# Kernel tuning notes

Measured on AMD Instinct MI355X. Metric: run time of the kernel, lower is better.

Reference implementation:

```python
import math
import jax, jax.numpy as jnp
import numpy as np

NEG = -1e10


def _rope_cos_sin(T, head_dim, dtype):
    # theta_i = 10000^(-2*(i-1)/dim), i=1..dim/2  ->  j=0..dim/2-1: 10000^(-2j/dim)
    j = jnp.arange(head_dim // 2, dtype=jnp.float32)
    inv_freq = 1.0 / (10000.0 ** (2.0 * j / head_dim))
    t = jnp.arange(T, dtype=jnp.float32)
    ang = t[:, None] * inv_freq[None, :]          # [T, hd/2]
    return jnp.cos(ang).astype(dtype), jnp.sin(ang).astype(dtype)


def _apply_rope(x, cos, sin):
    # x: [B, H, T, hd]; complex multiply (cos + i sin) * (x0 + i x1)
    B, H, T, hd = x.shape
    xr = x.reshape(B, H, T, hd // 2, 2)
    x0, x1 = xr[..., 0], xr[..., 1]
    c = cos[None, None]  # [1,1,T,hd/2]
    s = sin[None, None]
    o0 = c * x0 - s * x1
    o1 = s * x0 + c * x1
    return jnp.stack([o0, o1], axis=-1).reshape(B, H, T, hd)


def setup_inputs() -> dict:
    key = jax.random.key(0)
    ks = jax.random.split(key, 9)
    B, T, C = 2, 2048, 1024
    std = 0.02
    return {
        "x": jax.random.normal(ks[0], (B, T, C), jnp.float32),
        "Wq": jax.random.normal(ks[1], (C, C), jnp.float32) * std,
        "bq": jnp.zeros((C,), jnp.float32),
        "Wk": jax.random.normal(ks[2], (C, C), jnp.float32) * std,
        "bk": jnp.zeros((C,), jnp.float32),
        "Wv": jax.random.normal(ks[3], (C, C), jnp.float32) * std,
        "bv": jnp.zeros((C,), jnp.float32),
        "Wp": jax.random.normal(ks[4], (C, C), jnp.float32) * std,
        "bp": jnp.zeros((C,), jnp.float32),
    }


def reference(x, Wq, bq, Wk, bk, Wv, bv, Wp, bp):
    B, T, C = x.shape
    H = 16
    hd = C // H

    def heads(y):  # [B,T,C] -> [B,H,T,hd]
        return y.reshape(B, T, H, hd).transpose(0, 2, 1, 3)

    q = heads(x @ Wq.T + bq)
    k = heads(x @ Wk.T + bk)
    v = heads(x @ Wv.T + bv)

    cos, sin = _rope_cos_sin(T, hd, x.dtype)
    q = _apply_rope(q, cos, sin)
    k = _apply_rope(k, cos, sin)

    att = jnp.einsum('bhqd,bhkd->bhqk', q, k) * (1.0 / math.sqrt(hd))
    causal = jnp.tril(jnp.ones((T, T), bool))
    att = jnp.where(causal[None, None], att, jnp.asarray(NEG, att.dtype))
    att = jax.nn.softmax(att, axis=-1)

    y = jnp.einsum('bhqk,bhkd->bhqd', att, v)
    y = y.transpose(0, 2, 1, 3).reshape(B, T, C)
    return y @ Wp.T + bp
```

## Files before the change

kernel.cpp:

```cpp
#include <hip/hip_runtime.h>
#include <math.h>

typedef unsigned short u16;
typedef unsigned int u32;
typedef unsigned long long u64;
typedef __attribute__((ext_vector_type(8))) short short8;
typedef __attribute__((ext_vector_type(4))) float f32x4;
typedef __attribute__((ext_vector_type(4))) u16 u16x4;
typedef __attribute__((ext_vector_type(2))) u32 u32x2;
typedef __attribute__((ext_vector_type(4))) u32 u32x4;

#define AS1 __attribute__((address_space(1)))
#define AS3 __attribute__((address_space(3)))

#define QSCALE 0.18033688011112042f

__device__ __forceinline__ u16 f2bf(float f) {
  union { float f; u32 i; } u; u.f = f;
  u32 r = u.i + 0x7FFFu + ((u.i >> 16) & 1u);
  return (u16)(r >> 16);
}

__device__ __forceinline__ u32 pk_bf16(float a, float b) {
  u32 r;
  asm volatile("v_cvt_pk_bf16_f32 %0, %1, %2" : "=v"(r) : "v"(a), "v"(b));
  return r;
}

__device__ __forceinline__ void gl_lds16(const void* g, void* l) {
  __builtin_amdgcn_global_load_lds((const AS1 u32*)g, (AS3 u32*)l, 16, 0, 0);
}

#define MFMA32(a, b, c) __builtin_amdgcn_mfma_f32_16x16x32_bf16(a, b, c, 0, 0, 0)

__global__ void cvt_all(const float* __restrict__ x,
                        const float* __restrict__ Wq, const float* __restrict__ Wk,
                        const float* __restrict__ Wv, const float* __restrict__ Wp,
                        u16* __restrict__ xb,
                        u16* __restrict__ Wqb, u16* __restrict__ Wkb,
                        u16* __restrict__ Wvb, u16* __restrict__ Wpb,
                        float* __restrict__ cosT, float* __restrict__ sinT,
                        int n4x, int n4tot) {
  int i = blockIdx.x * 256 + threadIdx.x;
  if (i >= n4tot) {
    int k = i - n4tot;
    int t = k >> 5, j = k & 31;
    float inv = powf(10000.0f, -(float)j / 32.0f);
    float ang = (float)t * inv;
    cosT[k] = cosf(ang);
    sinT[k] = sinf(ang);
    return;
  }
  const float* src; u16* dst; int off;
  if (i < n4x) { src = x; dst = xb; off = i; }
  else {
    int wi = i - n4x;
    int sel = wi >> 18;
    off = wi & ((1 << 18) - 1);
    src = sel == 0 ? Wq : sel == 1 ? Wk : sel == 2 ? Wv : Wp;
    dst = sel == 0 ? Wqb : sel == 1 ? Wkb : sel == 2 ? Wvb : Wpb;
  }
  float4 v = ((const float4*)src)[off];
  u16x4 o = { f2bf(v.x), f2bf(v.y), f2bf(v.z), f2bf(v.w) };
  ((u16x4*)dst)[off] = o;
}

__global__ __launch_bounds__(256, 3) void gemm_qkv(
    const u16* __restrict__ xb,
    const u16* __restrict__ Wqb, const u16* __restrict__ Wkb, const u16* __restrict__ Wvb,
    const float* __restrict__ bq, const float* __restrict__ bk, const float* __restrict__ bv,
    const float* __restrict__ cosT, const float* __restrict__ sinT,
    u16* __restrict__ Qb, u16* __restrict__ Kb, u16* __restrict__ Vb) {
  const int K = 1024, N = 1024;
  __shared__ __attribute__((aligned(16))) u16 As[128 * 64];
  __shared__ __attribute__((aligned(16))) u16 Bs[128 * 64];
  const int tid = threadIdx.x;
  const int lane = tid & 63;
  const int hi = lane >> 4, cc = lane & 15;
  const int w = tid >> 6, wm = w >> 1, wn = w & 1;

  const int lin = blockIdx.x + 24 * blockIdx.y;
  const int a_ = lin & 7;
  const int m_ = lin >> 3;
  const int c_ = a_ * 3 + (m_ % 3);
  const int sel = c_ >> 3;
  const int row0 = (m_ / 3) * 128, col0 = (c_ & 7) * 128;

  const u16* W = sel == 0 ? Wqb : sel == 1 ? Wkb : Wvb;
  const float* bias = sel == 0 ? bq : sel == 1 ? bk : bv;
  u16* Out = sel == 0 ? Qb : sel == 1 ? Kb : Vb;

  const int lr = tid >> 3;
  const int lkb = (((tid & 7) ^ (lr & 7)) * 8);
  const u16* Ag = xb + (size_t)(row0 + lr) * K + lkb;
  const u16* Wg = W + (size_t)(col0 + lr) * K + lkb;

  f32x4 acc[4][4];
#pragma unroll
  for (int m = 0; m < 4; ++m)
#pragma unroll
    for (int n = 0; n < 4; ++n) acc[m][n] = f32x4{0.f, 0.f, 0.f, 0.f};

  for (int k0 = 0; k0 < K; k0 += 64) {
    __syncthreads();
#pragma unroll
    for (int j = 0; j < 4; ++j) {
      gl_lds16(Ag + (size_t)j * 32 * K + k0, As + j * 2048 + tid * 8);
      gl_lds16(Wg + (size_t)j * 32 * K + k0, Bs + j * 2048 + tid * 8);
    }
    __syncthreads();
    short8 a[2][4], b[2][4];
#pragma unroll
    for (int kk = 0; kk < 2; ++kk) {
#pragma unroll
      for (int m = 0; m < 4; ++m)
        a[kk][m] = *(const short8*)(As + (wm * 64 + m * 16 + cc) * 64 +
                                    (((kk * 4 + hi) ^ (cc & 7)) * 8));
#pragma unroll
      for (int n = 0; n < 4; ++n)
        b[kk][n] = *(const short8*)(Bs + (wn * 64 + n * 16 + cc) * 64 +
                                    (((kk * 4 + hi) ^ (cc & 7)) * 8));
    }
#pragma unroll
    for (int kk = 0; kk < 2; ++kk)
#pragma unroll
      for (int m = 0; m < 4; ++m)
#pragma unroll
        for (int n = 0; n < 4; ++n)
          acc[m][n] = MFMA32(a[kk][m], b[kk][n], acc[m][n]);
  }

  if (sel < 2) {
    const float qs = (sel == 0) ? QSCALE : 1.0f;
#pragma unroll
    for (int n = 0; n < 4; ++n) {
      const int col = col0 + wn * 64 + n * 16 + cc;
      const int j = (col & 63) >> 1;
      const float bb = bias[col];
#pragma unroll
      for (int m = 0; m < 4; ++m) {
        const int rw = row0 + wm * 64 + m * 16 + hi * 4;
#pragma unroll
        for (int r = 0; r < 4; ++r) {
          const int row = rw + r;
          const int t = row & 2047;
          float v = acc[m][n][r] + bb;
          float pv = __shfl_xor(v, 1);
          float c = cosT[t * 32 + j], s = sinT[t * 32 + j];
          float oo = (cc & 1) ? (s * pv + c * v) : (c * v - s * pv);
          Out[(size_t)row * N + col] = f2bf(oo * qs);
        }
      }
    }
  } else {
#pragma unroll
    for (int n = 0; n < 4; ++n) {
      const int col = col0 + wn * 64 + n * 16 + cc;
      const float bb = bias[col];
#pragma unroll
      for (int m = 0; m < 4; ++m) {
        const int rw = row0 + wm * 64 + m * 16 + hi * 4;
#pragma unroll
        for (int r = 0; r < 4; ++r)
          Out[(size_t)(rw + r) * N + col] = f2bf(acc[m][n][r] + bb);
      }
    }
  }
}

__global__ __launch_bounds__(512, 4) void flash_mfma(
    const u16* __restrict__ Qb, const u16* __restrict__ Kb,
    const u16* __restrict__ Vb, u16* __restrict__ Yb) {
  const int T = 2048, C = 1024;
  __shared__ __attribute__((aligned(16))) u16 Ks[64 * 64];
  __shared__ __attribute__((aligned(16))) u16 Vt[64 * 64];
  __shared__ __attribute__((aligned(16))) u16 Ps[8][16 * 64];

  const int tid = threadIdx.x;
  const int lane = tid & 63;
  const int hi = lane >> 4, cc = lane & 15;
  const int hi4 = hi * 4;
  const int w = tid >> 6;
  const int wl = w & 3;
  const int isB = w >> 2;

  const int lin = blockIdx.x + 16 * blockIdx.y;
  const int bh  = (lin & 7) * 4 + ((lin >> 3) & 3);
  const int qtA = lin >> 5;
  const int qtB = 31 - qtA;
  const int qtW = isB ? qtB : qtA;
  const size_t hbase = (size_t)(bh >> 4) * T * C + (size_t)(bh & 15) * 64;
  const int q0w = qtW * 64 + wl * 16;

  short8 qa0, qa1;
  {
    const u16* qp = Qb + hbase + (size_t)(q0w + cc) * C + hi * 8;
    qa0 = *(const short8*)qp;
    qa1 = *(const short8*)(qp + 32);
  }

  f32x4 o[4];
#pragma unroll
  for (int nt = 0; nt < 4; ++nt) o[nt] = f32x4{0.f, 0.f, 0.f, 0.f};
  float mrow = -1e30f, lsum = 0.f;

  const int krow = tid >> 3, kcol = (tid & 7) * 8;
  const int vd0 = (tid & 31) * 2, vkey0 = (tid >> 5) * 4;
  const u16* kgp = Kb + hbase + (size_t)krow * C + kcol;
  const u16* vgp = Vb + hbase + (size_t)vkey0 * C + vd0;

  short8 kr0;
  u32 vr_[4];

  auto LOADT = [&](int kt) {
    const size_t off = (size_t)(kt * 64) * C;
    kr0 = *(const short8*)(kgp + off);
#pragma unroll
    for (int j = 0; j < 4; ++j)
      vr_[j] = *(const u32*)(vgp + off + (size_t)j * C);
  };

  char* KsB = (char*)Ks;
  char* VtB = (char*)Vt;
  char* PsW = (char*)(Ps[w]);

  auto WRITET = [&]() {
    const int kb = krow * 128 + kcol * 2;
    const int ksw = (krow & 7) << 4;
    *(short8*)(KsB + (kb ^ ksw)) = kr0;
    u32 lo0 = (vr_[0] & 0xFFFFu) | (vr_[1] << 16);
    u32 lo1 = (vr_[2] & 0xFFFFu) | (vr_[3] << 16);
    u32 hh0 = (vr_[0] >> 16) | (vr_[1] & 0xFFFF0000u);
    u32 hh1 = (vr_[2] >> 16) | (vr_[3] & 0xFFFF0000u);
    const int d1 = vd0 + 1;
    u32x2 vlo = {lo0, lo1};
    u32x2 vhi = {hh0, hh1};
    *(u32x2*)(VtB + ((vd0 * 128 + vkey0 * 2) ^ ((vd0 & 7) << 4))) = vlo;
    *(u32x2*)(VtB + ((d1 * 128 + vkey0 * 2) ^ ((d1 & 7) << 4))) = vhi;
  };

  const int ksw2 = (cc & 7) << 4;

  LOADT(0);
  WRITET();
  LOADT(1);
  __syncthreads();

  for (int kt = 0; kt <= qtB; ++kt) {
    const bool act = (kt <= qtW);
    if (act) {
      short8 kf[4][2];
#pragma unroll
      for (int nt = 0; nt < 4; ++nt) {
        const int kb = (nt * 16 + cc) * 128 + hi * 16;
        kf[nt][0] = *(const short8*)(KsB + (kb ^ ksw2));
        kf[nt][1] = *(const short8*)(KsB + ((kb + 64) ^ ksw2));
      }

      f32x4 s[4];
#pragma unroll
      for (int nt = 0; nt < 4; ++nt) {
        f32x4 z = f32x4{0.f, 0.f, 0.f, 0.f};
        z = MFMA32(kf[nt][0], qa0, z);
        z = MFMA32(kf[nt][1], qa1, z);
        s[nt] = z;
      }

      if (kt == qtW) {
        const int qloc = wl * 16 + cc;
#pragma unroll
        for (int nt = 0; nt < 4; ++nt)
#pragma unroll
          for (int r = 0; r < 4; ++r)
            if (nt * 16 + hi4 + r > qloc) s[nt][r] = -1e30f;
      }

      float tm = s[0][0];
#pragma unroll
      for (int nt = 0; nt < 4; ++nt)
#pragma unroll
        for (int r = 0; r < 4; ++r) tm = fmaxf(tm, s[nt][r]);
      tm = fmaxf(tm, __shfl_xor(tm, 16));
      tm = fmaxf(tm, __shfl_xor(tm, 32));
      const bool need = tm > mrow + 8.0f;
      float corr = 1.0f;
      if (need) { corr = exp2f(mrow - tm); mrow = tm; }
      float psum = 0.f;
#pragma unroll
      for (int nt = 0; nt < 4; ++nt) {
        float e0 = exp2f(s[nt][0] - mrow);
        float e1 = exp2f(s[nt][1] - mrow);
        float e2 = exp2f(s[nt][2] - mrow);
        float e3 = exp2f(s[nt][3] - mrow);
        psum += (e0 + e1) + (e2 + e3);
        u32 pr[2] = { pk_bf16(e0, e1), pk_bf16(e2, e3) };
        *(u64*)(PsW + ((cc * 128 + nt * 32 + hi * 8) ^ ksw2)) = *(const u64*)pr;
      }
      psum += __shfl_xor(psum, 16);
      psum += __shfl_xor(psum, 32);
      lsum = lsum * corr + psum;
      if (__any(need)) {
#pragma unroll
        for (int nt = 0; nt < 4; ++nt) o[nt] *= corr;
      }

#pragma unroll
      for (int kc = 0; kc < 2; ++kc) {
        short8 pa = *(const short8*)(PsW + ((cc * 128 + kc * 64 + hi * 16) ^ ksw2));
#pragma unroll
        for (int nt = 0; nt < 4; ++nt) {
          short8 vb = *(const short8*)(VtB + (((nt * 16 + cc) * 128 + kc * 64 + hi * 16) ^ ksw2));
          o[nt] = MFMA32(vb, pa, o[nt]);
        }
      }
    }

    if (kt < qtB) {
      __syncthreads();
      WRITET();
      if (kt + 1 < qtB) LOADT(kt + 2);
      __syncthreads();
    }
  }

  const float ivl = 1.0f / lsum;
#pragma unroll
  for (int nt = 0; nt < 4; ++nt) {
    u16x4 y = { f2bf(o[nt][0] * ivl), f2bf(o[nt][1] * ivl),
                f2bf(o[nt][2] * ivl), f2bf(o[nt][3] * ivl) };
    *(u16x4*)(Yb + hbase + (size_t)(q0w + cc) * C + nt * 16 + hi4) = y;
  }
}

__global__ __launch_bounds__(256, 2) void gemm_proj(
    const u16* __restrict__ A, const u16* __restrict__ W,
    const float* __restrict__ bias, float* __restrict__ Out) {
  const int K = 1024, N = 1024;
  __shared__ __attribute__((aligned(16))) u16 As[128 * 64];
  __shared__ __attribute__((aligned(16))) u16 Bs[64 * 64];
  const int tid = threadIdx.x;
  const int lane = tid & 63;
  const int hi = lane >> 4, cc = lane & 15;
  const int w = tid >> 6, wm = w >> 1, wn = w & 1;

  const int lin = blockIdx.x + 16 * blockIdx.y;
  const int colt = (lin & 7) * 2 + ((lin >> 3) & 1);
  const int row0 = (lin >> 4) * 128, col0 = colt * 64;

  const int lr = tid >> 3;
  const int lkb = (((tid & 7) ^ (lr & 7)) * 8);
  const u16* Ag = A + (size_t)(row0 + lr) * K + lkb;
  const u16* Wg = W + (size_t)(col0 + lr) * K + lkb;

  f32x4 acc[4][2];
#pragma unroll
  for (int m = 0; m < 4; ++m)
#pragma unroll
    for (int n = 0; n < 2; ++n) acc[m][n] = f32x4{0.f, 0.f, 0.f, 0.f};

  for (int k0 = 0; k0 < K; k0 += 64) {
    __syncthreads();
#pragma unroll
    for (int j = 0; j < 4; ++j)
      gl_lds16(Ag + (size_t)j * 32 * K + k0, As + j * 2048 + tid * 8);
#pragma unroll
    for (int j = 0; j < 2; ++j)
      gl_lds16(Wg + (size_t)j * 32 * K + k0, Bs + j * 2048 + tid * 8);
    __syncthreads();
    short8 a[2][4], b[2][2];
#pragma unroll
    for (int kk = 0; kk < 2; ++kk) {
#pragma unroll
      for (int m = 0; m < 4; ++m)
        a[kk][m] = *(const short8*)(As + (wm * 64 + m * 16 + cc) * 64 +
                                    (((kk * 4 + hi) ^ (cc & 7)) * 8));
#pragma unroll
      for (int n = 0; n < 2; ++n)
        b[kk][n] = *(const short8*)(Bs + (wn * 32 + n * 16 + cc) * 64 +
                                    (((kk * 4 + hi) ^ (cc & 7)) * 8));
    }
#pragma unroll
    for (int kk = 0; kk < 2; ++kk)
#pragma unroll
      for (int m = 0; m < 4; ++m)
#pragma unroll
        for (int n = 0; n < 2; ++n)
          acc[m][n] = MFMA32(a[kk][m], b[kk][n], acc[m][n]);
  }

#pragma unroll
  for (int n = 0; n < 2; ++n) {
    const int col = col0 + wn * 32 + n * 16 + cc;
    const float bb = bias[col];
#pragma unroll
    for (int m = 0; m < 4; ++m) {
      const int rw = row0 + wm * 64 + m * 16 + hi * 4;
#pragma unroll
      for (int r = 0; r < 4; ++r)
        Out[(size_t)(rw + r) * N + col] = acc[m][n][r] + bb;
    }
  }
}

extern "C" void kernel_launch(void* const* d_in, const int* in_sizes, int n_in,
                              void* d_out, int out_size, void* d_ws, size_t ws_size,
                              hipStream_t stream) {
  const float* x  = (const float*)d_in[0];
  const float* Wq = (const float*)d_in[1];
  const float* bq = (const float*)d_in[2];
  const float* Wk = (const float*)d_in[3];
  const float* bk = (const float*)d_in[4];
  const float* Wv = (const float*)d_in[5];
  const float* bv = (const float*)d_in[6];
  const float* Wp = (const float*)d_in[7];
  const float* bp = (const float*)d_in[8];
  float* out = (float*)d_out;

  const int B = 2, T = 2048, C = 1024;
  const int M = B * T;
  const size_t MC = (size_t)M * C;
  const size_t CC = (size_t)C * C;

  char* p = (char*)d_ws;
  u16* xb  = (u16*)p;  p += MC * 2;
  u16* Wqb = (u16*)p;  p += CC * 2;
  u16* Wkb = (u16*)p;  p += CC * 2;
  u16* Wvb = (u16*)p;  p += CC * 2;
  u16* Wpb = (u16*)p;  p += CC * 2;
  u16* Qbb = (u16*)p;  p += MC * 2;
  u16* Kbb = (u16*)p;  p += MC * 2;
  u16* Vbb = (u16*)p;  p += MC * 2;
  float* cosT = (float*)p; p += (size_t)T * 32 * 4;
  float* sinT = (float*)p; p += (size_t)T * 32 * 4;

  const int n4x = (int)(MC / 4);
  const int n4tot = n4x + 4 * (int)(CC / 4);
  const int ntot = n4tot + T * 32;
  cvt_all<<<(ntot + 255) / 256, 256, 0, stream>>>(x, Wq, Wk, Wv, Wp,
                                                  xb, Wqb, Wkb, Wvb, Wpb,
                                                  cosT, sinT, n4x, n4tot);

  dim3 gq(24, M / 128);
  gemm_qkv<<<gq, 256, 0, stream>>>(xb, Wqb, Wkb, Wvb, bq, bk, bv, cosT, sinT, Qbb, Kbb, Vbb);

  dim3 fg(16, B * 16);
  flash_mfma<<<fg, 512, 0, stream>>>(Qbb, Kbb, Vbb, xb);

  dim3 gp(C / 64, M / 128);
  gemm_proj<<<gp, 256, 0, stream>>>(xb, Wpb, bp, out);
}
```

Baseline: 114.7 us.

## Keep softmax probabilities in registers and feed PV via 16x16x16 MFMA

Drops the per-wave LDS staging buffer for the probability tile. The bf16-packed exponentials stay in registers and become the A operand of 16x16x16 bf16 MFMAs for the P·V product, with the output layout transposed. Rescale factors and final normalisation are now fetched with cross-lane shuffles, and stores become scalar 2-byte writes. The change removes LDS writes and reads of P and their latency, but doubles the PV MFMA count at half depth, adds shuffles and less coalesced output stores, and lowers the launch-bound occupancy hint from 4 to 3.

Result: no change. 114.9 us (+0.1%).

```diff
diff --git a/kernel.cpp b/kernel.cpp
--- a/kernel.cpp
+++ b/kernel.cpp
@@ -5,6 +5,7 @@
 typedef unsigned int u32;
 typedef unsigned long long u64;
 typedef __attribute__((ext_vector_type(8))) short short8;
+typedef __attribute__((ext_vector_type(4))) short short4v;
 typedef __attribute__((ext_vector_type(4))) float f32x4;
 typedef __attribute__((ext_vector_type(4))) u16 u16x4;
 typedef __attribute__((ext_vector_type(2))) u32 u32x2;
@@ -32,6 +33,18 @@
 }
 
 #define MFMA32(a, b, c) __builtin_amdgcn_mfma_f32_16x16x32_bf16(a, b, c, 0, 0, 0)
+
+__device__ __forceinline__ f32x4 mfma16(short4v a, short4v b, f32x4 c) {
+#if __has_builtin(__builtin_amdgcn_mfma_f32_16x16x16_bf16)
+  return __builtin_amdgcn_mfma_f32_16x16x16_bf16(a, b, c, 0, 0, 0);
+#elif __has_builtin(__builtin_amdgcn_mfma_f32_16x16x16bf16_1k)
+  return __builtin_amdgcn_mfma_f32_16x16x16bf16_1k(a, b, c, 0, 0, 0);
+#else
+  f32x4 d = c;
+  asm("v_mfma_f32_16x16x16_bf16 %0, %1, %2, %0" : "+v"(d) : "v"(a), "v"(b));
+  return d;
+#endif
+}
 
 __global__ void cvt_all(const float* __restrict__ x,
                         const float* __restrict__ Wq, const float* __restrict__ Wk,
@@ -168,13 +181,12 @@
   }
 }
 
-__global__ __launch_bounds__(512, 4) void flash_mfma(
+__global__ __launch_bounds__(512, 3) void flash_mfma(
     const u16* __restrict__ Qb, const u16* __restrict__ Kb,
     const u16* __restrict__ Vb, u16* __restrict__ Yb) {
   const int T = 2048, C = 1024;
   __shared__ __attribute__((aligned(16))) u16 Ks[64 * 64];
   __shared__ __attribute__((aligned(16))) u16 Vt[64 * 64];
-  __shared__ __attribute__((aligned(16))) u16 Ps[8][16 * 64];
 
   const int tid = threadIdx.x;
   const int lane = tid & 63;
@@ -201,7 +213,7 @@
 
   f32x4 o[4];
 #pragma unroll
-  for (int nt = 0; nt < 4; ++nt) o[nt] = f32x4{0.f, 0.f, 0.f, 0.f};
+  for (int dc = 0; dc < 4; ++dc) o[dc] = f32x4{0.f, 0.f, 0.f, 0.f};
   float mrow = -1e30f, lsum = 0.f;
 
   const int krow = tid >> 3, kcol = (tid & 7) * 8;
@@ -222,7 +234,6 @@
 
   char* KsB = (char*)Ks;
   char* VtB = (char*)Vt;
-  char* PsW = (char*)(Ps[w]);
 
   auto WRITET = [&]() {
     const int kb = krow * 128 + kcol * 2;
@@ -249,20 +260,15 @@
   for (int kt = 0; kt <= qtB; ++kt) {
     const bool act = (kt <= qtW);
     if (act) {
-      short8 kf[4][2];
+      f32x4 s[4];
 #pragma unroll
       for (int nt = 0; nt < 4; ++nt) {
         const int kb = (nt * 16 + cc) * 128 + hi * 16;
-        kf[nt][0] = *(const short8*)(KsB + (kb ^ ksw2));
-        kf[nt][1] = *(const short8*)(KsB + ((kb + 64) ^ ksw2));
-      }
-
-      f32x4 s[4];
-#pragma unroll
-      for (int nt = 0; nt < 4; ++nt) {
+        short8 kf0 = *(const short8*)(KsB + (kb ^ ksw2));
+        short8 kf1 = *(const short8*)(KsB + ((kb + 64) ^ ksw2));
         f32x4 z = f32x4{0.f, 0.f, 0.f, 0.f};
-        z = MFMA32(kf[nt][0], qa0, z);
-        z = MFMA32(kf[nt][1], qa1, z);
+        z = MFMA32(kf0, qa0, z);
+        z = MFMA32(kf1, qa1, z);
         s[nt] = z;
       }
 
@@ -285,6 +291,8 @@
       const bool need = tm > mrow + 8.0f;
       float corr = 1.0f;
       if (need) { corr = exp2f(mrow - tm); mrow = tm; }
+
+      short4v pa[4];
       float psum = 0.f;
 #pragma unroll
       for (int nt = 0; nt < 4; ++nt) {
@@ -293,26 +301,32 @@
         float e2 = exp2f(s[nt][2] - mrow);
         float e3 = exp2f(s[nt][3] - mrow);
         psum += (e0 + e1) + (e2 + e3);
-        u32 pr[2] = { pk_bf16(e0, e1), pk_bf16(e2, e3) };
-        *(u64*)(PsW + ((cc * 128 + nt * 32 + hi * 8) ^ ksw2)) = *(const u64*)pr;
+        union { u32 u[2]; short4v v; } pu;
+        pu.u[0] = pk_bf16(e0, e1);
+        pu.u[1] = pk_bf16(e2, e3);
+        pa[nt] = pu.v;
       }
       psum += __shfl_xor(psum, 16);
       psum += __shfl_xor(psum, 32);
       lsum = lsum * corr + psum;
+
       if (__any(need)) {
-#pragma unroll
-        for (int nt = 0; nt < 4; ++nt) o[nt] *= corr;
-      }
-
-#pragma unroll
-      for (int kc = 0; kc < 2; ++kc) {
-        short8 pa = *(const short8*)(PsW + ((cc * 128 + kc * 64 + hi * 16) ^ ksw2));
-#pragma unroll
-        for (int nt = 0; nt < 4; ++nt) {
-          short8 vb = *(const short8*)(VtB + (((nt * 16 + cc) * 128 + kc * 64 + hi * 16) ^ ksw2));
-          o[nt] = MFMA32(vb, pa, o[nt]);
+        f32x4 cv;
+        cv[0] = __shfl(corr, hi4 + 0);
+        cv[1] = __shfl(corr, hi4 + 1);
+        cv[2] = __shfl(corr, hi4 + 2);
+        cv[3] = __shfl(corr, hi4 + 3);
+#pragma unroll
+        for (int dc = 0; dc < 4; ++dc) o[dc] *= cv;
+      }
+
+#pragma unroll
+      for (int nt = 0; nt < 4; ++nt)
+#pragma unroll
+        for (int dc = 0; dc < 4; ++dc) {
+          short4v vb = *(const short4v*)(VtB + (((dc * 16 + cc) * 128 + nt * 32 + hi * 8) ^ ksw2));
+          o[dc] = mfma16(pa[nt], vb, o[dc]);
         }
-      }
     }
 
     if (kt < qtB) {
@@ -323,13 +337,16 @@
     }
   }
 
-  const float ivl = 1.0f / lsum;
-#pragma unroll
-  for (int nt = 0; nt < 4; ++nt) {
-    u16x4 y = { f2bf(o[nt][0] * ivl), f2bf(o[nt][1] * ivl),
-                f2bf(o[nt][2] * ivl), f2bf(o[nt][3] * ivl) };
-    *(u16x4*)(Yb + hbase + (size_t)(q0w + cc) * C + nt * 16 + hi4) = y;
-  }
+  f32x4 iv;
+  iv[0] = 1.0f / __shfl(lsum, hi4 + 0);
+  iv[1] = 1.0f / __shfl(lsum, hi4 + 1);
+  iv[2] = 1.0f / __shfl(lsum, hi4 + 2);
+  iv[3] = 1.0f / __shfl(lsum, hi4 + 3);
+#pragma unroll
+  for (int dc = 0; dc < 4; ++dc)
+#pragma unroll
+    for (int r = 0; r < 4; ++r)
+      Yb[hbase + (size_t)(q0w + hi4 + r) * C + dc * 16 + cc] = f2bf(o[dc][r] * iv[r]);
 }
 
 __global__ __launch_bounds__(256, 2) void gemm_proj(
```
